# Kernel tuning notes

Measured on AMD Instinct MI355X. Metric: run time of the kernel, lower is better.

## Reference

```python
import jax, jax.numpy as jnp
import numpy as np

B, S, D, H, O, E, K = 8, 2048, 768, 3072, 768, 8, 2
LN_EPS = 1e-5


def setup_inputs() -> dict:
    key = jax.random.key(0)
    ks = jax.random.split(key, 8)
    x = jax.random.normal(ks[0], (B, S, D), dtype=jnp.float32)
    router_w = jax.random.normal(ks[1], (D, E), dtype=jnp.float32) * 0.02
    router_b = jnp.zeros((E,), dtype=jnp.float32)
    w1 = jax.random.normal(ks[2], (E, D, H), dtype=jnp.float32) * 0.02
    b1 = jnp.zeros((E, H), dtype=jnp.float32)
    w2 = jax.random.normal(ks[3], (E, H, O), dtype=jnp.float32) * 0.02
    b2 = jnp.zeros((E, O), dtype=jnp.float32)
    ln_g = jnp.ones((O,), dtype=jnp.float32)
    ln_b = jnp.zeros((O,), dtype=jnp.float32)
    return {"x": x, "router_w": router_w, "router_b": router_b,
            "w1": w1, "b1": b1, "w2": w2, "b2": b2,
            "ln_g": ln_g, "ln_b": ln_b}


def _layernorm(y, g, b):
    mu = jnp.mean(y, axis=-1, keepdims=True)
    var = jnp.mean(jnp.square(y - mu), axis=-1, keepdims=True)
    return (y - mu) * jax.lax.rsqrt(var + LN_EPS) * g + b


def reference(x, router_w, router_b, w1, b1, w2, b2, ln_g, ln_b):
    # Router (NoisyTopKRouter, eval mode: no noise): top-k gate over expert logits
    logits = jnp.einsum('bsd,de->bse', x, router_w) + router_b   # [B,S,E]
    top_vals, top_idx = jax.lax.top_k(logits, K)                 # [B,S,K]
    routing_weights = jax.nn.softmax(top_vals, axis=-1)          # [B,S,K]

    out = jnp.zeros((B, S, O), dtype=x.dtype)
    for e in range(E):
        # per-token combined weight for this expert (0 if not routed)
        w_e = jnp.sum(routing_weights * (top_idx == e), axis=-1)  # [B,S]
        # dense per-expert feedforward on ALL tokens (as in original loop)
        h = jax.nn.gelu(jnp.einsum('bsd,dh->bsh', x, w1[e]) + b1[e])
        y = jnp.einsum('bsh,ho->bso', h, w2[e]) + b2[e]
        out = out + y * w_e[..., None]
    return _layernorm(out, ln_g, ln_b)
```

## Files before the change

### kernel.cpp

```cpp
#include <hip/hip_runtime.h>
#include <hip/hip_bf16.h>
#include <stdint.h>

#define Bq  8
#define Sq  2048
#define Dq  768
#define Hq  3072
#define Oq  768
#define Eq  8
#define Mq  (Bq*Sq)
#define LN_EPS 1e-5f
#define MAX_T256 (Mq/128 + 16)

typedef unsigned short u16;
typedef __attribute__((ext_vector_type(4))) float f32x4;
typedef __attribute__((ext_vector_type(8))) __bf16 bf16x8;

static __device__ __forceinline__ u16 f2bf(float f) {
  __hip_bfloat16 h = __float2bfloat16(f);
  return __builtin_bit_cast(u16, h);
}
static __device__ __forceinline__ float bf2f(u16 h) {
  uint32_t u = (uint32_t)h << 16;
  return __builtin_bit_cast(float, u);
}

static __device__ __forceinline__ float gelu_f(float x) {
  float u = 0.7978845608028654f * x * (1.0f + 0.044715f * x * x);
  float e = __expf(2.0f * u);
  float t = 1.0f - 2.0f / (e + 1.0f);
  return 0.5f * x * (1.0f + t);
}

typedef const __attribute__((address_space(1))) void* gas_t;
typedef __attribute__((address_space(3))) void* las_t;
static __device__ __forceinline__ void gload16(const void* g, void* l) {
  __builtin_amdgcn_global_load_lds((gas_t)g, (las_t)l, 16, 0, 0);
}

__global__ __launch_bounds__(256) void router_cvt_kernel(
    const float* __restrict__ x, const float* __restrict__ rw,
    const float* __restrict__ rb, u16* __restrict__ Xbf,
    int* __restrict__ tok_seg, float2* __restrict__ tok_w,
    int* __restrict__ cnt)
{
  if (blockIdx.x == 0 && threadIdx.x < 16) cnt[threadIdx.x] = 0;

  __shared__ float rwT[Eq * Dq];
  for (int i = threadIdx.x; i < Eq * Dq; i += 256)
    rwT[(i & 7) * Dq + (i >> 3)] = rw[i];
  __syncthreads();

  int wid = threadIdx.x >> 6;
  int lane = threadIdx.x & 63;
  int token = blockIdx.x * 4 + wid;
  const float4* xrow = (const float4*)(x + (size_t)token * Dq);
  ushort4* orow = (ushort4*)(Xbf + (size_t)token * Dq);

  float acc[Eq];
#pragma unroll
  for (int e = 0; e < Eq; e++) acc[e] = 0.f;

#pragma unroll
  for (int it = 0; it < Dq / 256; it++) {
    int d4 = it * 64 + lane;
    float4 xv = xrow[d4];
    ushort4 o;
    o.x = f2bf(xv.x); o.y = f2bf(xv.y); o.z = f2bf(xv.z); o.w = f2bf(xv.w);
    orow[d4] = o;
    int d = d4 * 4;
#pragma unroll
    for (int e = 0; e < Eq; e++) {
      float4 wv = *(const float4*)&rwT[e * Dq + d];
      acc[e] += xv.x * wv.x + xv.y * wv.y + xv.z * wv.z + xv.w * wv.w;
    }
  }
#pragma unroll
  for (int e = 0; e < Eq; e++) {
    float v = acc[e];
#pragma unroll
    for (int off = 32; off; off >>= 1) v += __shfl_xor(v, off);
    acc[e] = v;
  }
  if (lane == 0) {
    float v1 = -1e30f, v2 = -1e30f; int i1 = 0, i2 = 0;
#pragma unroll
    for (int e = 0; e < Eq; e++) {
      float v = acc[e] + rb[e];
      if (v > v1)      { v2 = v1; i2 = i1; v1 = v; i1 = e; }
      else if (v > v2) { v2 = v;  i2 = e; }
    }
    float ex = expf(v2 - v1);
    float wa = 1.f / (1.f + ex);
    float wb = ex / (1.f + ex);
    tok_seg[token] = i1 | ((8 + i2) << 8);
    tok_w[token] = make_float2(wa, wb);
  }
}

__global__ __launch_bounds__(256) void scatter_build(
    const int* __restrict__ tok_seg, const float2* __restrict__ tok_w,
    int* __restrict__ cnt, int* __restrict__ seg_tok, float* __restrict__ seg_wgt,
    int2* __restrict__ tok_pos)
{
  __shared__ int histA[16], histB[16], base[16];
  int t = threadIdx.x;
  if (t < 16) { histA[t] = 0; histB[t] = 0; }
  __syncthreads();
  int token = blockIdx.x * 256 + t;
  int sp = tok_seg[token];
  float2 wv = tok_w[token];
  int s0 = sp & 0xff, s1 = sp >> 8;
  atomicAdd(&histA[s0], 1);
  atomicAdd(&histA[s1], 1);
  __syncthreads();
  if (t < 16) base[t] = atomicAdd(&cnt[t], histA[t]);
  __syncthreads();
  int p0 = base[s0] + atomicAdd(&histB[s0], 1);
  seg_tok[(size_t)s0 * Mq + p0] = token;
  seg_wgt[(size_t)s0 * Mq + p0] = wv.x;
  int p1 = base[s1] + atomicAdd(&histB[s1], 1);
  seg_tok[(size_t)s1 * Mq + p1] = token;
  seg_wgt[(size_t)s1 * Mq + p1] = wv.y;
  tok_pos[token] = make_int2(s0 | (p0 << 4), s1 | (p1 << 4));
}

__global__ __launch_bounds__(256) void transpose_cvt2(
    const float* __restrict__ w1, u16* __restrict__ W1T,
    const float* __restrict__ w2, u16* __restrict__ W2T)
{
  __shared__ float tile[32][33];
  const int which = blockIdx.z;
  const int R = which ? Hq : Dq;
  const int C = which ? Oq : Hq;
  const int NC = C / 32;
  const float* in = (which ? w2 : w1) + (size_t)blockIdx.y * R * C;
  u16* out = (which ? W2T : W1T) + (size_t)blockIdx.y * R * C;
  const int idx = blockIdx.x;
  const int c0 = (idx % NC) * 32, r0 = (idx / NC) * 32;
  int tx = threadIdx.x & 31, ty = threadIdx.x >> 5;
#pragma unroll
  for (int rr = 0; rr < 32; rr += 8)
    tile[rr + ty][tx] = in[(size_t)(r0 + rr + ty) * C + c0 + tx];
  __syncthreads();
#pragma unroll
  for (int rr = 0; rr < 32; rr += 8)
    out[(size_t)(c0 + rr + ty) * R + r0 + tx] = f2bf(tile[tx][rr + ty]);
}

__global__ __launch_bounds__(512, 2) void moe_gemm1(
    const u16* __restrict__ A, const u16* __restrict__ W,
    const float* __restrict__ bias, u16* __restrict__ Hout,
    const int* __restrict__ cnt, const int* __restrict__ seg_tok,
    int K, int N, int tile_lo)
{
  const int NP = N / 256;
  const int lid = (int)blockIdx.x + NP * (int)blockIdx.y;
  const int xcd = lid & 7, slot = lid >> 3;
  const int t_loc = xcd + 8 * (slot / NP);
  const int panel = slot % NP;

  const int t = tile_lo + t_loc;
  int pfx[16];
  {
    int tot = 0;
#pragma unroll
    for (int s2 = 0; s2 < 16; s2++) { pfx[s2] = tot; tot += (cnt[s2] + 255) >> 8; }
    if (t >= tot) return;
  }
  int seg = 0;
#pragma unroll
  for (int s2 = 1; s2 < 16; s2++) if (pfx[s2] <= t) seg = s2;
  const int e = seg & 7;
  const int segcnt = cnt[seg];
  const int ti = t - pfx[seg];
  const int lt = t_loc;

  __shared__ u16 smem[65536];
  const int tid  = threadIdx.x;
  const int lane = tid & 63;
  const int wid  = tid >> 6;
  const int wr   = wid >> 2, wc = wid & 3;
  const int lrow = lane & 15, kgrp = lane >> 4;
  const int gcx0 = ((kgrp)     ^ (lrow & 7)) * 8;
  const int gcx1 = ((4 + kgrp) ^ (lrow & 7)) * 8;

  f32x4 acc[8][4];
#pragma unroll
  for (int m = 0; m < 8; m++)
#pragma unroll
    for (int n = 0; n < 4; n++) acc[m][n] = (f32x4){0.f, 0.f, 0.f, 0.f};

  const int srow = tid >> 3;
  const int swz  = ((tid & 7) ^ (srow & 7)) * 8;
  const u16 *pA00, *pA01, *pA10, *pA11, *pB00, *pB01, *pB10, *pB11;
  {
    int sr;
    sr = ti * 256 +   0 +  0 + srow;
    pA00 = A + (size_t)((sr < segcnt) ? seg_tok[(size_t)seg * Mq + sr] : 0) * K + swz;
    sr = ti * 256 +   0 + 64 + srow;
    pA01 = A + (size_t)((sr < segcnt) ? seg_tok[(size_t)seg * Mq + sr] : 0) * K + swz;
    sr = ti * 256 + 128 +  0 + srow;
    pA10 = A + (size_t)((sr < segcnt) ? seg_tok[(size_t)seg * Mq + sr] : 0) * K + swz;
    sr = ti * 256 + 128 + 64 + srow;
    pA11 = A + (size_t)((sr < segcnt) ? seg_tok[(size_t)seg * Mq + sr] : 0) * K + swz;
    const u16* Wb = W + (size_t)e * K * N;
    pB00 = Wb + (size_t)(panel * 256 +   0 +  0 + srow) * K + swz;
    pB01 = Wb + (size_t)(panel * 256 +   0 + 64 + srow) * K + swz;
    pB10 = Wb + (size_t)(panel * 256 + 128 +  0 + srow) * K + swz;
    pB11 = Wb + (size_t)(panel * 256 + 128 + 64 + srow) * K + swz;
  }

#define STG(base, h, P0, P1)                               \
  do {                                                     \
    gload16(P0, &smem[(base) + (h) * 8192 + tid * 8]);     \
    gload16(P1, &smem[(base) + (h) * 8192 + 4096 + tid * 8]); \
    P0 += 64; P1 += 64;                                    \
  } while (0)

  const int NKT = K / 64;
  STG(0, 0, pA00, pA01); STG(0, 1, pA10, pA11);
  STG(32768, 0, pB00, pB01); STG(32768, 1, pB10, pB11);

  bf16x8 bfr[4][2];
  for (int kt = 0; kt < NKT; ++kt) {
    const int s = kt & 1;
    const int sA = s * 16384, sB = 32768 + s * 16384;
    const int dA = (s ^ 1) * 16384, dB = 32768 + (s ^ 1) * 16384;
    const bool more = (kt + 1 < NKT);
    const int abase = wr * 128 + lrow;
    const int bbase = wc * 64 + lrow;

    if (more) {
      STG(dA, 0, pA00, pA01);
      asm volatile("s_waitcnt vmcnt(2)" ::: "memory");
    } else {
      asm volatile("s_waitcnt vmcnt(0)" ::: "memory");
    }
    __builtin_amdgcn_s_barrier();
    __builtin_amdgcn_sched_barrier(0);
#pragma unroll
    for (int n = 0; n < 4; n++) {
      bfr[n][0] = *(const bf16x8*)&smem[sB + (bbase + n * 16) * 64 + gcx0];
      bfr[n][1] = *(const bf16x8*)&smem[sB + (bbase + n * 16) * 64 + gcx1];
    }
    {
      bf16x8 a00 = *(const bf16x8*)&smem[sA + (abase +  0) * 64 + gcx0];
      bf16x8 a01 = *(const bf16x8*)&smem[sA + (abase +  0) * 64 + gcx1];
      bf16x8 a10 = *(const bf16x8*)&smem[sA + (abase + 16) * 64 + gcx0];
      bf16x8 a11 = *(const bf16x8*)&smem[sA + (abase + 16) * 64 + gcx1];
      __builtin_amdgcn_s_setprio(1);
#pragma unroll
      for (int n = 0; n < 4; n++) {
        acc[0][n] = __builtin_amdgcn_mfma_f32_16x16x32_bf16(a00, bfr[n][0], acc[0][n], 0, 0, 0);
        acc[0][n] = __builtin_amdgcn_mfma_f32_16x16x32_bf16(a01, bfr[n][1], acc[0][n], 0, 0, 0);
        acc[1][n] = __builtin_amdgcn_mfma_f32_16x16x32_bf16(a10, bfr[n][0], acc[1][n], 0, 0, 0);
        acc[1][n] = __builtin_amdgcn_mfma_f32_16x16x32_bf16(a11, bfr[n][1], acc[1][n], 0, 0, 0);
      }
      __builtin_amdgcn_s_setprio(0);
    }
    __builtin_amdgcn_sched_barrier(0);
    __builtin_amdgcn_s_barrier();

#define PHASE(q, STGSTMT)                                                     \
    do {                                                                      \
      bf16x8 a00 = *(const bf16x8*)&smem[sA + (abase + (2*(q))    * 16) * 64 + gcx0]; \
      bf16x8 a01 = *(const bf16x8*)&smem[sA + (abase + (2*(q))    * 16) * 64 + gcx1]; \
      bf16x8 a10 = *(const bf16x8*)&smem[sA + (abase + (2*(q)+1)  * 16) * 64 + gcx0]; \
      bf16x8 a11 = *(const bf16x8*)&smem[sA + (abase + (2*(q)+1)  * 16) * 64 + gcx1]; \
      if (more) { STGSTMT; }                                                  \
      __builtin_amdgcn_s_setprio(1);                                          \
      _Pragma("unroll")                                                       \
      for (int n = 0; n < 4; n++) {                                           \
        acc[2*(q)][n]   = __builtin_amdgcn_mfma_f32_16x16x32_bf16(a00, bfr[n][0], acc[2*(q)][n], 0, 0, 0);   \
        acc[2*(q)][n]   = __builtin_amdgcn_mfma_f32_16x16x32_bf16(a01, bfr[n][1], acc[2*(q)][n], 0, 0, 0);   \
        acc[2*(q)+1][n] = __builtin_amdgcn_mfma_f32_16x16x32_bf16(a10, bfr[n][0], acc[2*(q)+1][n], 0, 0, 0); \
        acc[2*(q)+1][n] = __builtin_amdgcn_mfma_f32_16x16x32_bf16(a11, bfr[n][1], acc[2*(q)+1][n], 0, 0, 0); \
      }                                                                       \
      __builtin_amdgcn_s_setprio(0);                                          \
      __builtin_amdgcn_sched_barrier(0);                                      \
      __builtin_amdgcn_s_barrier();                                           \
    } while (0)

    PHASE(1, STG(dA, 1, pA10, pA11));
    PHASE(2, STG(dB, 0, pB00, pB01));
    PHASE(3, STG(dB, 1, pB10, pB11));
#undef PHASE
  }
#undef STG

  {
    const int rb = wr * 128, cb = wc * 64;
#pragma unroll
    for (int n = 0; n < 4; n++) {
      int cc = cb + n * 16 + lrow;
      float bv = bias[(size_t)e * N + panel * 256 + cc];
#pragma unroll
      for (int m = 0; m < 8; m++)
#pragma unroll
        for (int j = 0; j < 4; j++) {
          int rr = rb + m * 16 + kgrp * 4 + j;
          smem[rr * 256 + cc] = f2bf(gelu_f(acc[m][n][j] + bv));
        }
    }
    __syncthreads();
    const int r = tid >> 5, c8 = (tid & 31) * 8;
    u16* gdst = Hout + (size_t)(lt * 256) * N + (size_t)panel * 256;
#pragma unroll
    for (int it2 = 0; it2 < 16; ++it2) {
      int rr = it2 * 16 + r;
      *(uint4*)(gdst + (size_t)rr * N + c8) = *(const uint4*)&smem[rr * 256 + c8];
    }
  }
}

__global__ __launch_bounds__(256) void moe_gemm2(
    const u16* __restrict__ A, const u16* __restrict__ W,
    const float* __restrict__ bias, u16* __restrict__ Ybuf,
    const int* __restrict__ cnt, const int* __restrict__ seg_tok,
    const float* __restrict__ seg_wgt, int K, int N, int tile_lo)
{
  const int NP = N / 128;
  const int lid = (int)blockIdx.x + NP * (int)blockIdx.y;
  const int xcd = lid & 7, slot = lid >> 3;
  const int t2 = xcd + 8 * (slot / NP);
  const int panel = slot % NP;

  const int t256 = tile_lo + (t2 >> 1);
  int pfx[16];
  {
    int tot = 0;
#pragma unroll
    for (int s2 = 0; s2 < 16; s2++) { pfx[s2] = tot; tot += (cnt[s2] + 255) >> 8; }
    if (t256 >= tot) return;
  }
  int seg = 0;
#pragma unroll
  for (int s2 = 1; s2 < 16; s2++) if (pfx[s2] <= t256) seg = s2;
  const int e = seg & 7;
  const int segcnt = cnt[seg];
  const int ti = (t256 - pfx[seg]) * 2 + (t2 & 1);
  const int lt = t2;

  __shared__ u16 smem[16384];
  const int tid  = threadIdx.x;
  const int lane = tid & 63;
  const int wid  = tid >> 6;
  const int wr   = wid >> 1, wc = wid & 1;
  const int lrow = lane & 15, kgrp = lane >> 4;
  const int kx   = kgrp ^ ((lrow >> 1) & 3);
  const int n0 = panel * 128;

  f32x4 acc[4][4];
#pragma unroll
  for (int m = 0; m < 4; m++)
#pragma unroll
    for (int n = 0; n < 4; n++) acc[m][n] = (f32x4){0.f, 0.f, 0.f, 0.f};

  const int r0 = tid >> 2;
  const int kc = (((tid & 3) ^ ((tid >> 3) & 3)) * 8);
  const u16* gA0 = A + (size_t)(lt * 128 + r0) * K + kc;
  const u16* gA1 = gA0 + (size_t)64 * K;
  const u16* gB = W + (size_t)e * K * N + (size_t)(n0 + r0) * K + kc;
  const size_t rowskipB = (size_t)64 * K;
  const int lofs = tid * 8;

  auto stage = [&](int b) {
    gload16(gA0, &smem[b * 4096 + lofs]);
    gload16(gA1, &smem[b * 4096 + lofs + 2048]);
    gload16(gB,            &smem[8192 + b * 4096 + lofs]);
    gload16(gB + rowskipB, &smem[8192 + b * 4096 + lofs + 2048]);
    gA0 += 32; gA1 += 32; gB += 32;
  };

  const int NIT = K / 32;
  stage(0);
  for (int it = 0; it < NIT; ++it) {
    const int cur = it & 1;
    if (it + 1 < NIT) {
      stage(cur ^ 1);
      asm volatile("s_waitcnt vmcnt(4)" ::: "memory");
    } else {
      asm volatile("s_waitcnt vmcnt(0)" ::: "memory");
    }
    __builtin_amdgcn_s_barrier();
    __builtin_amdgcn_sched_barrier(0);
    bf16x8 a[4], b[4];
#pragma unroll
    for (int m = 0; m < 4; m++)
      a[m] = *(const bf16x8*)&smem[cur * 4096 + (wr * 64 + m * 16 + lrow) * 32 + kx * 8];
#pragma unroll
    for (int n = 0; n < 4; n++)
      b[n] = *(const bf16x8*)&smem[8192 + cur * 4096 + (wc * 64 + n * 16 + lrow) * 32 + kx * 8];
#pragma unroll
    for (int m = 0; m < 4; m++)
#pragma unroll
      for (int n = 0; n < 4; n++)
        acc[m][n] = __builtin_amdgcn_mfma_f32_16x16x32_bf16(a[m], b[n], acc[m][n], 0, 0, 0);
    __builtin_amdgcn_sched_barrier(0);
    __builtin_amdgcn_s_barrier();
  }

  {
    const int rbase = wr * 64;
    const int cbase = wc * 64;
    float bv[4];
#pragma unroll
    for (int n = 0; n < 4; n++)
      bv[n] = bias[(size_t)e * N + n0 + cbase + n * 16 + lrow];
#pragma unroll
    for (int m = 0; m < 4; m++)
#pragma unroll
      for (int j = 0; j < 4; j++) {
        int r = rbase + m * 16 + kgrp * 4 + j;
        int i = ti * 128 + r;
        float w = (i < segcnt) ? seg_wgt[(size_t)seg * Mq + i] : 0.f;
#pragma unroll
        for (int n = 0; n < 4; n++) {
          int c = cbase + n * 16 + lrow;
          smem[r * 128 + c] = f2bf((acc[m][n][j] + bv[n]) * w);
        }
      }
    __syncthreads();
    const size_t gi0 = (size_t)t256 * 256 + (size_t)(t2 & 1) * 128;
    const int r = tid >> 4, c8 = (tid & 15) * 8;
    u16* gdst = Ybuf + gi0 * Oq + n0;
#pragma unroll
    for (int p = 0; p < 8; ++p) {
      int rr = p * 16 + r;
      *(uint4*)(gdst + (size_t)rr * Oq + c8) = *(const uint4*)&smem[rr * 128 + c8];
    }
  }
}

__global__ __launch_bounds__(256) void ln2_kernel(
    const u16* __restrict__ Ybuf, const int* __restrict__ cnt,
    const int2* __restrict__ tok_pos, const float* __restrict__ g,
    const float* __restrict__ b, float* __restrict__ out)
{
  int wid = threadIdx.x >> 6, lane = threadIdx.x & 63;
  int token = blockIdx.x * 4 + wid;
  int pfx[16];
  {
    int tot = 0;
#pragma unroll
    for (int s = 0; s < 16; s++) { pfx[s] = tot; tot += (cnt[s] + 255) >> 8; }
  }
  int2 pp = tok_pos[token];
  size_t gi0 = (size_t)pfx[pp.x & 15] * 256 + (pp.x >> 4);
  size_t gi1 = (size_t)pfx[pp.y & 15] * 256 + (pp.y >> 4);
  const u16* r0 = Ybuf + gi0 * Oq;
  const u16* r1 = Ybuf + gi1 * Oq;

  float v[12];
  {
    uint4 w0 = *(const uint4*)(r0 + lane * 8);
    uint4 w1 = *(const uint4*)(r1 + lane * 8);
    uint32_t u0[4] = {w0.x, w0.y, w0.z, w0.w};
    uint32_t u1[4] = {w1.x, w1.y, w1.z, w1.w};
#pragma unroll
    for (int k = 0; k < 4; k++) {
      v[2 * k]     = bf2f((u16)(u0[k] & 0xffff)) + bf2f((u16)(u1[k] & 0xffff));
      v[2 * k + 1] = bf2f((u16)(u0[k] >> 16))    + bf2f((u16)(u1[k] >> 16));
    }
    ushort4 t0 = *(const ushort4*)(r0 + 512 + lane * 4);
    ushort4 t1 = *(const ushort4*)(r1 + 512 + lane * 4);
    v[8]  = bf2f(t0.x) + bf2f(t1.x);
    v[9]  = bf2f(t0.y) + bf2f(t1.y);
    v[10] = bf2f(t0.z) + bf2f(t1.z);
    v[11] = bf2f(t0.w) + bf2f(t1.w);
  }

  float s = 0.f;
#pragma unroll
  for (int i = 0; i < 12; i++) s += v[i];
#pragma unroll
  for (int off = 32; off; off >>= 1) s += __shfl_xor(s, off);
  float mu = s * (1.0f / Oq);
  float q = 0.f;
#pragma unroll
  for (int i = 0; i < 12; i++) { float d = v[i] - mu; q += d * d; }
#pragma unroll
  for (int off = 32; off; off >>= 1) q += __shfl_xor(q, off);
  float inv = rsqrtf(q * (1.0f / Oq) + LN_EPS);

  float* orow = out + (size_t)token * Oq;
  {
    float4 g0 = *(const float4*)(g + lane * 8);
    float4 g1 = *(const float4*)(g + lane * 8 + 4);
    float4 b0 = *(const float4*)(b + lane * 8);
    float4 b1 = *(const float4*)(b + lane * 8 + 4);
    float4 o0, o1;
    o0.x = (v[0] - mu) * inv * g0.x + b0.x;
    o0.y = (v[1] - mu) * inv * g0.y + b0.y;
    o0.z = (v[2] - mu) * inv * g0.z + b0.z;
    o0.w = (v[3] - mu) * inv * g0.w + b0.w;
    o1.x = (v[4] - mu) * inv * g1.x + b1.x;
    o1.y = (v[5] - mu) * inv * g1.y + b1.y;
    o1.z = (v[6] - mu) * inv * g1.z + b1.z;
    o1.w = (v[7] - mu) * inv * g1.w + b1.w;
    *(float4*)(orow + lane * 8) = o0;
    *(float4*)(orow + lane * 8 + 4) = o1;
    float4 g2v = *(const float4*)(g + 512 + lane * 4);
    float4 b2v = *(const float4*)(b + 512 + lane * 4);
    float4 o2;
    o2.x = (v[8]  - mu) * inv * g2v.x + b2v.x;
    o2.y = (v[9]  - mu) * inv * g2v.y + b2v.y;
    o2.z = (v[10] - mu) * inv * g2v.z + b2v.z;
    o2.w = (v[11] - mu) * inv * g2v.w + b2v.w;
    *(float4*)(orow + 512 + lane * 4) = o2;
  }
}

extern "C" void kernel_launch(void* const* d_in, const int* in_sizes, int n_in,
                              void* d_out, int out_size, void* d_ws, size_t ws_size,
                              hipStream_t stream)
{
  const float* x    = (const float*)d_in[0];
  const float* rw   = (const float*)d_in[1];
  const float* rb   = (const float*)d_in[2];
  const float* w1   = (const float*)d_in[3];
  const float* b1   = (const float*)d_in[4];
  const float* w2   = (const float*)d_in[5];
  const float* b2   = (const float*)d_in[6];
  const float* ln_g = (const float*)d_in[7];
  const float* ln_b = (const float*)d_in[8];
  float* out = (float*)d_out;

  char* ws = (char*)d_ws;
  size_t off = 0;
  auto alloc = [&](size_t bytes) {
    void* p = ws + off;
    off += (bytes + 255) & ~(size_t)255;
    return p;
  };
  int*    cnt     = (int*)alloc(16 * 4);
  int*    tok_seg = (int*)alloc((size_t)Mq * 4);
  float2* tok_w   = (float2*)alloc((size_t)Mq * 8);
  int2*   tok_pos = (int2*)alloc((size_t)Mq * 8);
  int*    seg_tok = (int*)alloc((size_t)16 * Mq * 4);
  float*  seg_wgt = (float*)alloc((size_t)16 * Mq * 4);
  u16* Xbf = (u16*)alloc((size_t)Mq * Dq * 2);
  u16* W1T = (u16*)alloc((size_t)Eq * Dq * Hq * 2);
  u16* W2T = (u16*)alloc((size_t)Eq * Hq * Oq * 2);
  u16* Ybuf = (u16*)alloc((size_t)MAX_T256 * 256 * Oq * 2);

  size_t remain = (ws_size > off) ? ws_size - off : 0;
  size_t tile_bytes = (size_t)256 * Hq * 2;
  long long wt = (long long)(remain / tile_bytes);
  if (wt > MAX_T256) wt = MAX_T256;
  wt &= ~7LL;
  if (wt < 8) wt = 8;
  int WT = (int)wt;
  u16* Hbuf = (u16*)alloc((size_t)WT * tile_bytes);

  router_cvt_kernel<<<Mq / 4, 256, 0, stream>>>(x, rw, rb, Xbf, tok_seg, tok_w, cnt);
  scatter_build<<<Mq / 256, 256, 0, stream>>>(tok_seg, tok_w, cnt, seg_tok, seg_wgt, tok_pos);
  transpose_cvt2<<<dim3((Dq / 32) * (Hq / 32), Eq, 2), 256, 0, stream>>>(
      w1, W1T, w2, W2T);

  for (int tl = 0; tl < MAX_T256; tl += WT) {
    int gx = MAX_T256 - tl; if (gx > WT) gx = WT;
    moe_gemm1<<<dim3(Hq / 256, gx), 512, 0, stream>>>(
        Xbf, W1T, b1, Hbuf, cnt, seg_tok, Dq, Hq, tl);
    moe_gemm2<<<dim3(Oq / 128, 2 * gx), 256, 0, stream>>>(
        Hbuf, W2T, b2, Ybuf, cnt, seg_tok, seg_wgt, Hq, Oq, tl);
  }
  ln2_kernel<<<Mq / 4, 256, 0, stream>>>(Ybuf, cnt, tok_pos, ln_g, ln_b, out);
}
```

Before: 625.2 us.

## Amortize router LDS load, vectorize weight transpose, deepen gemm2 K-step pipeline

The router kernel now handles 32 tokens per block instead of 4, so the 8x768 router-weight transpose into LDS is paid far less often. The weight transpose/convert kernel moves to 64x64 tiles with float4 loads and 16-byte packed bf16 stores, cutting the number of memory transactions. The gemm2 mainloop switches to K=64 steps with an XOR swizzle over 8 chunks and splits each step into four phases, staggering the next tile's global-to-LDS loads between MFMA groups and raising wave priority around the MFMAs. The gemm2 change doubles LDS use and adds extra barriers per K-step, which may lower occupancy.

New measurement: 636.4 us. Within noise of the previous version (+1.8%).

```diff
diff --git a/kernel.cpp b/kernel.cpp
--- a/kernel.cpp
+++ b/kernel.cpp
@@ -53,48 +53,51 @@
 
   int wid = threadIdx.x >> 6;
   int lane = threadIdx.x & 63;
-  int token = blockIdx.x * 4 + wid;
-  const float4* xrow = (const float4*)(x + (size_t)token * Dq);
-  ushort4* orow = (ushort4*)(Xbf + (size_t)token * Dq);
-
-  float acc[Eq];
-#pragma unroll
-  for (int e = 0; e < Eq; e++) acc[e] = 0.f;
-
-#pragma unroll
-  for (int it = 0; it < Dq / 256; it++) {
-    int d4 = it * 64 + lane;
-    float4 xv = xrow[d4];
-    ushort4 o;
-    o.x = f2bf(xv.x); o.y = f2bf(xv.y); o.z = f2bf(xv.z); o.w = f2bf(xv.w);
-    orow[d4] = o;
-    int d = d4 * 4;
+
+  for (int tt = 0; tt < 8; ++tt) {
+    int token = blockIdx.x * 32 + wid * 8 + tt;
+    const float4* xrow = (const float4*)(x + (size_t)token * Dq);
+    ushort4* orow = (ushort4*)(Xbf + (size_t)token * Dq);
+
+    float acc[Eq];
+#pragma unroll
+    for (int e = 0; e < Eq; e++) acc[e] = 0.f;
+
+#pragma unroll
+    for (int it = 0; it < Dq / 256; it++) {
+      int d4 = it * 64 + lane;
+      float4 xv = xrow[d4];
+      ushort4 o;
+      o.x = f2bf(xv.x); o.y = f2bf(xv.y); o.z = f2bf(xv.z); o.w = f2bf(xv.w);
+      orow[d4] = o;
+      int d = d4 * 4;
+#pragma unroll
+      for (int e = 0; e < Eq; e++) {
+        float4 wv = *(const float4*)&rwT[e * Dq + d];
+        acc[e] += xv.x * wv.x + xv.y * wv.y + xv.z * wv.z + xv.w * wv.w;
+      }
+    }
 #pragma unroll
     for (int e = 0; e < Eq; e++) {
-      float4 wv = *(const float4*)&rwT[e * Dq + d];
-      acc[e] += xv.x * wv.x + xv.y * wv.y + xv.z * wv.z + xv.w * wv.w;
-    }
-  }
-#pragma unroll
-  for (int e = 0; e < Eq; e++) {
-    float v = acc[e];
-#pragma unroll
-    for (int off = 32; off; off >>= 1) v += __shfl_xor(v, off);
-    acc[e] = v;
-  }
-  if (lane == 0) {
-    float v1 = -1e30f, v2 = -1e30f; int i1 = 0, i2 = 0;
-#pragma unroll
-    for (int e = 0; e < Eq; e++) {
-      float v = acc[e] + rb[e];
-      if (v > v1)      { v2 = v1; i2 = i1; v1 = v; i1 = e; }
-      else if (v > v2) { v2 = v;  i2 = e; }
-    }
-    float ex = expf(v2 - v1);
-    float wa = 1.f / (1.f + ex);
-    float wb = ex / (1.f + ex);
-    tok_seg[token] = i1 | ((8 + i2) << 8);
-    tok_w[token] = make_float2(wa, wb);
+      float v = acc[e];
+#pragma unroll
+      for (int off = 32; off; off >>= 1) v += __shfl_xor(v, off);
+      acc[e] = v;
+    }
+    if (lane == 0) {
+      float v1 = -1e30f, v2 = -1e30f; int i1 = 0, i2 = 0;
+#pragma unroll
+      for (int e = 0; e < Eq; e++) {
+        float v = acc[e] + rb[e];
+        if (v > v1)      { v2 = v1; i2 = i1; v1 = v; i1 = e; }
+        else if (v > v2) { v2 = v;  i2 = e; }
+      }
+      float ex = expf(v2 - v1);
+      float wa = 1.f / (1.f + ex);
+      float wb = ex / (1.f + ex);
+      tok_seg[token] = i1 | ((8 + i2) << 8);
+      tok_w[token] = make_float2(wa, wb);
+    }
   }
 }
 
@@ -125,27 +128,44 @@
   tok_pos[token] = make_int2(s0 | (p0 << 4), s1 | (p1 << 4));
 }
 
-__global__ __launch_bounds__(256) void transpose_cvt2(
+__global__ __launch_bounds__(256) void transpose_cvt64(
     const float* __restrict__ w1, u16* __restrict__ W1T,
     const float* __restrict__ w2, u16* __restrict__ W2T)
 {
-  __shared__ float tile[32][33];
+  __shared__ float tile[64][65];
   const int which = blockIdx.z;
   const int R = which ? Hq : Dq;
   const int C = which ? Oq : Hq;
-  const int NC = C / 32;
+  const int NC = C / 64;
   const float* in = (which ? w2 : w1) + (size_t)blockIdx.y * R * C;
   u16* out = (which ? W2T : W1T) + (size_t)blockIdx.y * R * C;
-  const int idx = blockIdx.x;
-  const int c0 = (idx % NC) * 32, r0 = (idx / NC) * 32;
-  int tx = threadIdx.x & 31, ty = threadIdx.x >> 5;
-#pragma unroll
-  for (int rr = 0; rr < 32; rr += 8)
-    tile[rr + ty][tx] = in[(size_t)(r0 + rr + ty) * C + c0 + tx];
+  const int c0 = ((int)blockIdx.x % NC) * 64;
+  const int r0 = ((int)blockIdx.x / NC) * 64;
+
+  const int fx = threadIdx.x & 15, rb = threadIdx.x >> 4;
+#pragma unroll
+  for (int rr = 0; rr < 64; rr += 16) {
+    float4 v = *(const float4*)&in[(size_t)(r0 + rr + rb) * C + c0 + fx * 4];
+    tile[rr + rb][fx * 4 + 0] = v.x;
+    tile[rr + rb][fx * 4 + 1] = v.y;
+    tile[rr + rb][fx * 4 + 2] = v.z;
+    tile[rr + rb][fx * 4 + 3] = v.w;
+  }
   __syncthreads();
-#pragma unroll
-  for (int rr = 0; rr < 32; rr += 8)
-    out[(size_t)(c0 + rr + ty) * R + r0 + tx] = f2bf(tile[tx][rr + ty]);
+  const int j = threadIdx.x & 7;
+#pragma unroll
+  for (int pass = 0; pass < 2; ++pass) {
+    int oc = (threadIdx.x >> 3) + pass * 32;
+    u16 vals[8];
+#pragma unroll
+    for (int k = 0; k < 8; ++k) vals[k] = f2bf(tile[j * 8 + k][oc]);
+    uint4 w;
+    w.x = vals[0] | ((uint32_t)vals[1] << 16);
+    w.y = vals[2] | ((uint32_t)vals[3] << 16);
+    w.z = vals[4] | ((uint32_t)vals[5] << 16);
+    w.w = vals[6] | ((uint32_t)vals[7] << 16);
+    *(uint4*)&out[(size_t)(c0 + oc) * R + r0 + j * 8] = w;
+  }
 }
 
 __global__ __launch_bounds__(512, 2) void moe_gemm1(
@@ -342,13 +362,14 @@
   const int ti = (t256 - pfx[seg]) * 2 + (t2 & 1);
   const int lt = t2;
 
-  __shared__ u16 smem[16384];
+  __shared__ u16 smem[32768];
   const int tid  = threadIdx.x;
   const int lane = tid & 63;
   const int wid  = tid >> 6;
   const int wr   = wid >> 1, wc = wid & 1;
   const int lrow = lane & 15, kgrp = lane >> 4;
-  const int kx   = kgrp ^ ((lrow >> 1) & 3);
+  const int gcx0 = ((kgrp)     ^ (lrow & 7)) * 8;
+  const int gcx1 = ((4 + kgrp) ^ (lrow & 7)) * 8;
   const int n0 = panel * 128;
 
   f32x4 acc[4][4];
@@ -357,48 +378,83 @@
 #pragma unroll
     for (int n = 0; n < 4; n++) acc[m][n] = (f32x4){0.f, 0.f, 0.f, 0.f};
 
-  const int r0 = tid >> 2;
-  const int kc = (((tid & 3) ^ ((tid >> 3) & 3)) * 8);
-  const u16* gA0 = A + (size_t)(lt * 128 + r0) * K + kc;
-  const u16* gA1 = gA0 + (size_t)64 * K;
-  const u16* gB = W + (size_t)e * K * N + (size_t)(n0 + r0) * K + kc;
-  const size_t rowskipB = (size_t)64 * K;
-  const int lofs = tid * 8;
-
-  auto stage = [&](int b) {
-    gload16(gA0, &smem[b * 4096 + lofs]);
-    gload16(gA1, &smem[b * 4096 + lofs + 2048]);
-    gload16(gB,            &smem[8192 + b * 4096 + lofs]);
-    gload16(gB + rowskipB, &smem[8192 + b * 4096 + lofs + 2048]);
-    gA0 += 32; gA1 += 32; gB += 32;
+  const int srow = tid >> 3;
+  const int swz  = ((tid & 7) ^ (srow & 7)) * 8;
+  const u16* gA[4];
+  const u16* gB[4];
+#pragma unroll
+  for (int c = 0; c < 4; c++) {
+    gA[c] = A + (size_t)(lt * 128 + c * 32 + srow) * K + swz;
+    gB[c] = W + (size_t)e * K * N + (size_t)(n0 + c * 32 + srow) * K + swz;
+  }
+  const int dofs = srow * 64 + (tid & 7) * 8;
+
+  auto stg2 = [&](int base, int h, const u16** P) {
+    gload16(P[2 * h],     &smem[base + (2 * h) * 2048 + dofs]);
+    gload16(P[2 * h + 1], &smem[base + (2 * h + 1) * 2048 + dofs]);
+    P[2 * h] += 64; P[2 * h + 1] += 64;
   };
 
-  const int NIT = K / 32;
-  stage(0);
-  for (int it = 0; it < NIT; ++it) {
-    const int cur = it & 1;
-    if (it + 1 < NIT) {
-      stage(cur ^ 1);
-      asm volatile("s_waitcnt vmcnt(4)" ::: "memory");
+  const int NIT = K / 64;
+  stg2(0, 0, gA); stg2(0, 1, gA);
+  stg2(16384, 0, gB); stg2(16384, 1, gB);
+
+  bf16x8 bfr[4][2];
+  for (int kt = 0; kt < NIT; ++kt) {
+    const int s = kt & 1;
+    const int sA = s * 8192, sB = 16384 + s * 8192;
+    const int dA = (s ^ 1) * 8192, dB = 16384 + (s ^ 1) * 8192;
+    const bool more = (kt + 1 < NIT);
+    const int abase = wr * 64 + lrow;
+    const int bbase = wc * 64 + lrow;
+
+    if (more) {
+      stg2(dA, 0, gA);
+      asm volatile("s_waitcnt vmcnt(2)" ::: "memory");
     } else {
       asm volatile("s_waitcnt vmcnt(0)" ::: "memory");
     }
     __builtin_amdgcn_s_barrier();
     __builtin_amdgcn_sched_barrier(0);
-    bf16x8 a[4], b[4];
-#pragma unroll
-    for (int m = 0; m < 4; m++)
-      a[m] = *(const bf16x8*)&smem[cur * 4096 + (wr * 64 + m * 16 + lrow) * 32 + kx * 8];
-#pragma unroll
-    for (int n = 0; n < 4; n++)
-      b[n] = *(const bf16x8*)&smem[8192 + cur * 4096 + (wc * 64 + n * 16 + lrow) * 32 + kx * 8];
-#pragma unroll
-    for (int m = 0; m < 4; m++)
-#pragma unroll
-      for (int n = 0; n < 4; n++)
-        acc[m][n] = __builtin_amdgcn_mfma_f32_16x16x32_bf16(a[m], b[n], acc[m][n], 0, 0, 0);
+#pragma unroll
+    for (int n = 0; n < 4; n++) {
+      bfr[n][0] = *(const bf16x8*)&smem[sB + (bbase + n * 16) * 64 + gcx0];
+      bfr[n][1] = *(const bf16x8*)&smem[sB + (bbase + n * 16) * 64 + gcx1];
+    }
+    {
+      bf16x8 a0 = *(const bf16x8*)&smem[sA + (abase + 0) * 64 + gcx0];
+      bf16x8 a1 = *(const bf16x8*)&smem[sA + (abase + 0) * 64 + gcx1];
+      __builtin_amdgcn_s_setprio(1);
+#pragma unroll
+      for (int n = 0; n < 4; n++) {
+        acc[0][n] = __builtin_amdgcn_mfma_f32_16x16x32_bf16(a0, bfr[n][0], acc[0][n], 0, 0, 0);
+        acc[0][n] = __builtin_amdgcn_mfma_f32_16x16x32_bf16(a1, bfr[n][1], acc[0][n], 0, 0, 0);
+      }
+      __builtin_amdgcn_s_setprio(0);
+    }
     __builtin_amdgcn_sched_barrier(0);
     __builtin_amdgcn_s_barrier();
+
+#define PHASE2(q, STGSTMT)                                                    \
+    do {                                                                      \
+      bf16x8 a0 = *(const bf16x8*)&smem[sA + (abase + (q) * 16) * 64 + gcx0]; \
+      bf16x8 a1 = *(const bf16x8*)&smem[sA + (abase + (q) * 16) * 64 + gcx1]; \
+      if (more) { STGSTMT; }                                                  \
+      __builtin_amdgcn_s_setprio(1);                                          \
+      _Pragma("unroll")                                                       \
+      for (int n = 0; n < 4; n++) {                                           \
+        acc[q][n] = __builtin_amdgcn_mfma_f32_16x16x32_bf16(a0, bfr[n][0], acc[q][n], 0, 0, 0); \
+        acc[q][n] = __builtin_amdgcn_mfma_f32_16x16x32_bf16(a1, bfr[n][1], acc[q][n], 0, 0, 0); \
+      }                                                                       \
+      __builtin_amdgcn_s_setprio(0);                                          \
+      __builtin_amdgcn_sched_barrier(0);                                      \
+      __builtin_amdgcn_s_barrier();                                           \
+    } while (0)
+
+    PHASE2(1, stg2(dA, 1, gA));
+    PHASE2(2, stg2(dB, 0, gB));
+    PHASE2(3, stg2(dB, 1, gB));
+#undef PHASE2
   }
 
   {
@@ -554,9 +610,9 @@
   int WT = (int)wt;
   u16* Hbuf = (u16*)alloc((size_t)WT * tile_bytes);
 
-  router_cvt_kernel<<<Mq / 4, 256, 0, stream>>>(x, rw, rb, Xbf, tok_seg, tok_w, cnt);
+  router_cvt_kernel<<<Mq / 32, 256, 0, stream>>>(x, rw, rb, Xbf, tok_seg, tok_w, cnt);
   scatter_build<<<Mq / 256, 256, 0, stream>>>(tok_seg, tok_w, cnt, seg_tok, seg_wgt, tok_pos);
-  transpose_cvt2<<<dim3((Dq / 32) * (Hq / 32), Eq, 2), 256, 0, stream>>>(
+  transpose_cvt64<<<dim3((Dq / 64) * (Hq / 64), Eq, 2), 256, 0, stream>>>(
       w1, W1T, w2, W2T);
 
   for (int tl = 0; tl < MAX_T256; tl += WT) {
```
